# Optimization experiments

Measured on AMD Instinct MI355X. Metric: run time of the kernel, lower is better.

## Reference

```python
import jax, jax.numpy as jnp
import numpy as np


def setup_inputs() -> dict:
    key = jax.random.key(0)
    P, B, S = 128, 128, 4096
    k1, k2, k3, k4 = jax.random.split(key, 4)
    # SPD inducing Gram K_ii
    A = jax.random.normal(k1, (P, 2 * P), jnp.float32)
    K_ii = A @ A.T / (2.0 * P) + 1e-2 * jnp.eye(P, dtype=jnp.float32)
    # cross-covariances [B, S, P]
    K_ti = jax.random.normal(k2, (B, S, P), jnp.float32) * 0.1
    # diagonal K_t must dominate the quadratic form so the Schur complement is positive
    Kii_inv = jnp.linalg.inv(K_ii)
    qf = jnp.einsum('bsp,pq,bsq->bs', K_ti, Kii_inv, K_ti)
    K_t = qf + jax.random.uniform(k3, (B, S), jnp.float32) + 0.1
    # learned parameters
    V = jax.random.normal(k4, (P, P), jnp.float32) / jnp.sqrt(P) + jnp.eye(P, dtype=jnp.float32)
    latent_Gscale = jnp.zeros((), jnp.float32)
    dof = 128
    return dict(K_ii=K_ii, K_ti=K_ti, K_t=K_t, V=V, latent_Gscale=latent_Gscale, dof=dof)


def reference(K_ii, K_ti, K_t, V, latent_Gscale, dof):
    P = K_ii.shape[0]
    ti = K_ti.reshape(-1, P)          # [N, P]
    tt = K_t.reshape(-1)              # [N]
    # pos_inv via Cholesky (SPD inverse)
    L = jnp.linalg.cholesky(K_ii)
    Kii_inv = jax.scipy.linalg.cho_solve((L, True), jnp.eye(P, dtype=K_ii.dtype))
    A = ti @ Kii_inv                  # Kti_inv_Kii_flat, [N, P]
    ktt_i = tt - jnp.sum(A * ti, -1)  # Schur complement diag
    # G = V V^T / P * exp(scale)
    G = (V @ V.T) / V.shape[1] * jnp.exp(latent_Gscale)
    Gti = A @ G                       # [N, P]
    gt = jnp.sum(Gti * A, -1) + ktt_i
    # objective: -0.5 * dof * (-(logdet G + logdet Kinv) + tr(Kinv G) - P)
    trace_term = jnp.sum(Kii_inv * G.T)
    logdet_G = jnp.linalg.slogdet(G)[1]
    logdet_Kinv = -2.0 * jnp.sum(jnp.log(jnp.diag(L)))
    obj = -0.5 * dof * (-(logdet_G + logdet_Kinv) + trace_term - P)
    Gii = G
    return (Gii, Gti.reshape(K_ti.shape), gt.reshape(K_t.shape), obj)
```

## Files before the change

kernel.cpp:

```cpp
#include <hip/hip_runtime.h>
#include <cstdint>

typedef __attribute__((ext_vector_type(8))) short short8;
typedef __attribute__((ext_vector_type(4))) float f32x4;

__device__ __forceinline__ unsigned short f2bf(float f) {
    uint32_t u = __builtin_bit_cast(uint32_t, f);
    u += 0x7FFFu + ((u >> 16) & 1u);
    return (unsigned short)(u >> 16);
}

#define SG_OFF   16384
#define SM1_OFF  32768
#define SY_OFF   49152
#define SX_OFF   65536
#define SD_OFF   81920

__global__ __launch_bounds__(256) void k0_G(
    const float* __restrict__ V, const float* __restrict__ gs,
    float* __restrict__ out)
{
    float* sG = out + SG_OFF;
    const float egs = expf(gs[0]) * (1.0f / 128.0f);
    const int ty = threadIdx.x >> 5, tx = threadIdx.x & 31;
    const int r = blockIdx.x * 8 + ty;
    const f32x4* V4 = (const f32x4*)V;
    f32x4 acc = {0.f, 0.f, 0.f, 0.f};
    for (int kq = 0; kq < 32; ++kq) {
        const f32x4 vr = V4[r * 32 + kq];
        #pragma unroll
        for (int e = 0; e < 4; ++e) {
            const f32x4 vc = V4[(tx * 4 + e) * 32 + kq];
            acc[e] += vr[0]*vc[0] + vr[1]*vc[1] + vr[2]*vc[2] + vr[3]*vc[3];
        }
    }
    acc *= egs;
    *(f32x4*)&out[r * 128 + tx * 4] = acc;
    *(f32x4*)&sG[r * 128 + tx * 4] = acc;
}

__global__ __launch_bounds__(512) void k1_factor(
    const float* __restrict__ Kii, float* __restrict__ out)
{
    __shared__ float colA[2][128], colB[2][128], rowX[2][128];
    __shared__ float sDk[128], sDg[128], sRed[4];

    const int tid = threadIdx.x;
    const int ty = tid >> 5, tx = tid & 31;
    const int I0 = ty * 8, J0 = tx * 4;
    const float* sG = out + SG_OFF;
    float* sX = out + SX_OFF;
    float* dbuf = out + SD_OFF;

    f32x4 rA[8], rB[8], rX[8];
    #pragma unroll
    for (int r = 0; r < 8; ++r) {
        rA[r] = *(const f32x4*)&Kii[(size_t)(I0 + r) * 128 + J0];
        rB[r] = *(const f32x4*)&sG[(I0 + r) * 128 + J0];
        f32x4 z = {0.f, 0.f, 0.f, 0.f};
        #pragma unroll
        for (int e = 0; e < 4; ++e) z[e] = (I0 + r == J0 + e) ? 1.0f : 0.0f;
        rX[r] = z;
    }
    if (tx == 0) {
        #pragma unroll
        for (int r = 0; r < 8; ++r) { colA[0][I0 + r] = rA[r][0]; colB[0][I0 + r] = rB[r][0]; }
    }
    if (ty == 0) {
        #pragma unroll
        for (int e = 0; e < 4; ++e) rowX[0][J0 + e] = rX[0][e];
    }
    __syncthreads();

    for (int k = 0; k < 127; ++k) {
        const int b = k & 1;
        const float dK = colA[b][k], dG = colB[b][k];
        const float rdK = 1.0f / dK, rdG = 1.0f / dG;
        if (tid == 0) { sDk[k] = dK; sDg[k] = dG; }

        f32x4 caj = *(const f32x4*)&colA[b][J0];
        f32x4 cbj = *(const f32x4*)&colB[b][J0];
        const f32x4 xj = *(const f32x4*)&rowX[b][J0];
        #pragma unroll
        for (int e = 0; e < 4; ++e)
            if (J0 + e <= k) { caj[e] = 0.0f; cbj[e] = 0.0f; }

        f32x4 ca0 = *(const f32x4*)&colA[b][I0];
        f32x4 ca1 = *(const f32x4*)&colA[b][I0 + 4];
        f32x4 cb0 = *(const f32x4*)&colB[b][I0];
        f32x4 cb1 = *(const f32x4*)&colB[b][I0 + 4];
        #pragma unroll
        for (int r = 0; r < 4; ++r) {
            if (I0 + r <= k)     { ca0[r] = 0.0f; cb0[r] = 0.0f; }
            if (I0 + 4 + r <= k) { ca1[r] = 0.0f; cb1[r] = 0.0f; }
        }

        if (I0 + 7 > k) {
            #pragma unroll
            for (int r = 0; r < 8; ++r) {
                const float am = (r < 4) ? ca0[r & 3] : ca1[r & 3];
                const float bm = (r < 4) ? cb0[r & 3] : cb1[r & 3];
                const float fA = am * rdK;
                const float fB = bm * rdG;
                rA[r] -= fA * caj;
                rB[r] -= fB * cbj;
                rX[r] -= fA * xj;
            }
        }

        const int kn = k + 1, bn = kn & 1;
        if (tx == (kn >> 2)) {
            const int es = kn & 3;
            #pragma unroll
            for (int ee = 0; ee < 4; ++ee) if (ee == es) {
                #pragma unroll
                for (int r = 0; r < 8; ++r) {
                    colA[bn][I0 + r] = rA[r][ee];
                    colB[bn][I0 + r] = rB[r][ee];
                }
            }
        }
        if (ty == (kn >> 3)) {
            const int rs = kn & 7;
            #pragma unroll
            for (int rr = 0; rr < 8; ++rr) if (rr == rs) {
                #pragma unroll
                for (int e = 0; e < 4; ++e) rowX[bn][J0 + e] = rX[rr][e];
            }
        }
        __syncthreads();
    }
    if (tid == 511) { sDk[127] = rA[7][3]; sDg[127] = rB[7][3]; }

    #pragma unroll
    for (int r = 0; r < 8; ++r)
        *(f32x4*)&sX[(I0 + r) * 128 + J0] = rX[r];
    __syncthreads();

    if (tid < 128) {
        dbuf[tid] = sDk[tid];
        float lk = logf(sDk[tid]);
        float lg = logf(sDg[tid]);
        #pragma unroll
        for (int o = 32; o > 0; o >>= 1) { lk += __shfl_xor(lk, o, 64); lg += __shfl_xor(lg, o, 64); }
        if ((tid & 63) == 0) { sRed[(tid >> 6) * 2] = lk; sRed[(tid >> 6) * 2 + 1] = lg; }
    }
    __syncthreads();
    if (tid == 0) {
        dbuf[128] = sRed[0] + sRed[2];
        dbuf[129] = sRed[1] + sRed[3];
    }
}

__global__ __launch_bounds__(256) void k2_M1(float* __restrict__ out)
{
    const float* sX = out + SX_OFF;
    const float* dbuf = out + SD_OFF;
    float* sM1 = out + SM1_OFF;
    __shared__ float srd[128];
    const int tid = threadIdx.x;
    if (tid < 128) srd[tid] = 1.0f / dbuf[tid];
    __syncthreads();
    const int ty = tid >> 5, tx = tid & 31;
    const int a = blockIdx.x * 8 + ty;
    const f32x4* X4 = (const f32x4*)sX;
    f32x4 acc = {0.f, 0.f, 0.f, 0.f};
    for (int k = a; k < 128; ++k) {
        const float xa = sX[k * 128 + a] * srd[k];
        acc += xa * X4[k * 32 + tx];
    }
    *(f32x4*)&sM1[a * 128 + tx * 4] = acc;
}

__global__ __launch_bounds__(256) void k3_Y(float* __restrict__ out, char* __restrict__ wsb)
{
    const float* sG = out + SG_OFF;
    const float* sM1 = out + SM1_OFF;
    float* sY = out + SY_OFF;
    float* dbuf = out + SD_OFF;
    const int tid = threadIdx.x;
    const int ty = tid >> 5, tx = tid & 31;
    const int c = blockIdx.x * 8 + ty;
    const f32x4* M14 = (const f32x4*)sM1;
    f32x4 acc = {0.f, 0.f, 0.f, 0.f};
    for (int m = 0; m < 128; ++m)
        acc += sG[c * 128 + m] * M14[m * 32 + tx];
    *(f32x4*)&sY[c * 128 + tx * 4] = acc;
    const uint32_t lo = (uint32_t)f2bf(acc[0]) | ((uint32_t)f2bf(acc[1]) << 16);
    const uint32_t hi = (uint32_t)f2bf(acc[2]) | ((uint32_t)f2bf(acc[3]) << 16);
    const uint32_t byteoff = (uint32_t)((c * 256 + tx * 8) ^ ((c & 7) << 4));
    *(uint2*)(wsb + byteoff) = make_uint2(lo, hi);
    float t;
    {
        const f32x4* G4 = (const f32x4*)sG;
        const int idx = blockIdx.x * 256 + tid;
        const f32x4 g = G4[idx], mm = M14[idx];
        t = g[0]*mm[0] + g[1]*mm[1] + g[2]*mm[2] + g[3]*mm[3];
    }
    #pragma unroll
    for (int o = 32; o > 0; o >>= 1) t += __shfl_xor(t, o, 64);
    __shared__ float sp[4];
    if ((tid & 63) == 0) sp[tid >> 6] = t;
    __syncthreads();
    if (tid == 0) dbuf[132 + blockIdx.x] = sp[0] + sp[1] + sp[2] + sp[3];
}

__global__ __launch_bounds__(256) void k4_Q(
    float* __restrict__ out, char* __restrict__ wsb, const int* __restrict__ dofp)
{
    const float* sM1 = out + SM1_OFF;
    const float* sY = out + SY_OFF;
    const float* dbuf = out + SD_OFF;
    const int tid = threadIdx.x;
    const int ty = tid >> 5, tx = tid & 31;
    const int c = blockIdx.x * 8 + ty;
    const f32x4* Y4 = (const f32x4*)sY;
    const f32x4* M14 = (const f32x4*)sM1;
    f32x4 acc = -M14[c * 32 + tx];
    for (int m = 0; m < 128; ++m)
        acc += sM1[c * 128 + m] * Y4[m * 32 + tx];
    const uint32_t lo = (uint32_t)f2bf(acc[0]) | ((uint32_t)f2bf(acc[1]) << 16);
    const uint32_t hi = (uint32_t)f2bf(acc[2]) | ((uint32_t)f2bf(acc[3]) << 16);
    const uint32_t byteoff = (uint32_t)((c * 256 + tx * 8) ^ ((c & 7) << 4));
    *(uint2*)(wsb + 32768 + byteoff) = make_uint2(lo, hi);
    if (blockIdx.x == 0 && tid == 0) {
        float trace = 0.0f;
        for (int i = 0; i < 16; ++i) trace += dbuf[132 + i];
        const float ldK = dbuf[128], ldG = dbuf[129];
        const float dof = (float)dofp[0];
        out[67649536] = -0.5f * dof * (-(ldG - ldK) + trace - 128.0f);
    }
}

__global__ __launch_bounds__(512) void main_kernel(
    const float* __restrict__ Kti, const float* __restrict__ Kt,
    const float* __restrict__ ws, float* __restrict__ Gti,
    float* __restrict__ gt)
{
    __shared__ __align__(16) char smem[65536];
    const int tid = threadIdx.x;
    const int lane = tid & 63, wid = tid >> 6;
    const int l15 = lane & 15, l4 = lane >> 4;
    const int brow = blockIdx.x * 256;
    const int wrow = wid * 32;

    const float* tbase = Kti + (size_t)(brow + wrow + l15) * 128;

    f32x4 t[4][4];
    #pragma unroll
    for (int kc = 0; kc < 4; ++kc) {
        const float* p0 = tbase + kc * 32 + l4 * 8;
        const float* p1 = p0 + 16 * 128;
        t[kc][0] = *(const f32x4*)p0;
        t[kc][1] = *(const f32x4*)(p0 + 4);
        t[kc][2] = *(const f32x4*)p1;
        t[kc][3] = *(const f32x4*)(p1 + 4);
    }

    {
        f32x4* s4 = (f32x4*)smem;
        const f32x4* w4 = (const f32x4*)ws;
        #pragma unroll
        for (int i = 0; i < 8; ++i) s4[tid + i * 512] = w4[tid + i * 512];
    }

    short8 a[4][2];
    #pragma unroll
    for (int kc = 0; kc < 4; ++kc) {
        a[kc][0] = { (short)f2bf(t[kc][0][0]), (short)f2bf(t[kc][0][1]), (short)f2bf(t[kc][0][2]), (short)f2bf(t[kc][0][3]),
                     (short)f2bf(t[kc][1][0]), (short)f2bf(t[kc][1][1]), (short)f2bf(t[kc][1][2]), (short)f2bf(t[kc][1][3]) };
        a[kc][1] = { (short)f2bf(t[kc][2][0]), (short)f2bf(t[kc][2][1]), (short)f2bf(t[kc][2][2]), (short)f2bf(t[kc][2][3]),
                     (short)f2bf(t[kc][3][0]), (short)f2bf(t[kc][3][1]), (short)f2bf(t[kc][3][2]), (short)f2bf(t[kc][3][3]) };
    }
    __syncthreads();

    f32x4 accW[2][8] = {};
    f32x4 accZ[2][8] = {};
    #pragma unroll
    for (int kc = 0; kc < 4; ++kc) {
        const int k0 = kc * 32 + l4 * 8;
        #pragma unroll
        for (int ct = 0; ct < 8; ++ct) {
            const int c = ct * 16 + l15;
            const int byteoff = (c * 256 + k0 * 2) ^ ((c & 7) << 4);
            const short8 bW = *(const short8*)(smem + byteoff);
            const short8 bQ = *(const short8*)(smem + 32768 + byteoff);
            accW[0][ct] = __builtin_amdgcn_mfma_f32_16x16x32_bf16(a[kc][0], bW, accW[0][ct], 0, 0, 0);
            accW[1][ct] = __builtin_amdgcn_mfma_f32_16x16x32_bf16(a[kc][1], bW, accW[1][ct], 0, 0, 0);
            accZ[0][ct] = __builtin_amdgcn_mfma_f32_16x16x32_bf16(a[kc][0], bQ, accZ[0][ct], 0, 0, 0);
            accZ[1][ct] = __builtin_amdgcn_mfma_f32_16x16x32_bf16(a[kc][1], bQ, accZ[1][ct], 0, 0, 0);
        }
    }

    #pragma unroll
    for (int rt = 0; rt < 2; ++rt) {
        #pragma unroll
        for (int r = 0; r < 4; ++r) {
            const int row = brow + wrow + rt * 16 + l4 * 4 + r;
            const float* trow = Kti + (size_t)row * 128;
            float p = 0.0f;
            #pragma unroll
            for (int ct = 0; ct < 8; ++ct) p += accZ[rt][ct][r] * trow[ct * 16 + l15];
            p += __shfl_xor(p, 1, 64);
            p += __shfl_xor(p, 2, 64);
            p += __shfl_xor(p, 4, 64);
            p += __shfl_xor(p, 8, 64);
            if (l15 == 0) gt[row] = Kt[row] + p;
        }
    }

    #pragma unroll
    for (int rt = 0; rt < 2; ++rt) {
        #pragma unroll
        for (int r = 0; r < 4; ++r) {
            float* grow = Gti + (size_t)(brow + wrow + rt * 16 + l4 * 4 + r) * 128 + l15;
            #pragma unroll
            for (int ct = 0; ct < 8; ++ct)
                grow[ct * 16] = accW[rt][ct][r];
        }
    }
}

extern "C" void kernel_launch(void* const* d_in, const int* in_sizes, int n_in,
                              void* d_out, int out_size, void* d_ws, size_t ws_size,
                              hipStream_t stream)
{
    const float* Kii = (const float*)d_in[0];
    const float* Kti = (const float*)d_in[1];
    const float* Kt  = (const float*)d_in[2];
    const float* V   = (const float*)d_in[3];
    const float* gs  = (const float*)d_in[4];
    const int*   dof = (const int*)d_in[5];
    float* out = (float*)d_out;
    float* ws  = (float*)d_ws;

    const int N = in_sizes[2];
    const int nblocks = N / 256;

    k0_G<<<16, 256, 0, stream>>>(V, gs, out);
    k1_factor<<<1, 512, 0, stream>>>(Kii, out);
    k2_M1<<<16, 256, 0, stream>>>(out);
    k3_Y<<<16, 256, 0, stream>>>(out, (char*)ws);
    k4_Q<<<16, 256, 0, stream>>>(out, (char*)ws, dof);
    main_kernel<<<nblocks, 512, 0, stream>>>(Kti, Kt, ws,
                                             out + 16384,
                                             out + 67125248);
}
```

Before: 305.5 us.

## Make main kernel persistent with 128-row tiles and register prefetch of next tile

The main kernel becomes a persistent grid of 512 blocks that loop over 128-row tiles. Each wave now handles 16 rows instead of 32, which halves the accumulator registers, and launch bounds request 4 blocks per CU. The next tile's K_ti rows are prefetched into registers while the MFMAs for the current tile run, and the 64KB weight copy into LDS happens once per block instead of once per 256 rows. The risks are the LDS budget limiting real occupancy below the requested 4 blocks, and the smaller per-wave tile lowering MFMA density.

```diff
diff --git a/kernel.cpp b/kernel.cpp
--- a/kernel.cpp
+++ b/kernel.cpp
@@ -232,30 +232,16 @@
     }
 }
 
-__global__ __launch_bounds__(512) void main_kernel(
+__global__ __launch_bounds__(512, 4) void main_kernel(
     const float* __restrict__ Kti, const float* __restrict__ Kt,
     const float* __restrict__ ws, float* __restrict__ Gti,
-    float* __restrict__ gt)
+    float* __restrict__ gt, int ntiles)
 {
     __shared__ __align__(16) char smem[65536];
     const int tid = threadIdx.x;
     const int lane = tid & 63, wid = tid >> 6;
     const int l15 = lane & 15, l4 = lane >> 4;
-    const int brow = blockIdx.x * 256;
-    const int wrow = wid * 32;
-
-    const float* tbase = Kti + (size_t)(brow + wrow + l15) * 128;
-
-    f32x4 t[4][4];
-    #pragma unroll
-    for (int kc = 0; kc < 4; ++kc) {
-        const float* p0 = tbase + kc * 32 + l4 * 8;
-        const float* p1 = p0 + 16 * 128;
-        t[kc][0] = *(const f32x4*)p0;
-        t[kc][1] = *(const f32x4*)(p0 + 4);
-        t[kc][2] = *(const f32x4*)p1;
-        t[kc][3] = *(const f32x4*)(p1 + 4);
-    }
+    const int wrow = wid * 16;
 
     {
         f32x4* s4 = (f32x4*)smem;
@@ -264,60 +250,79 @@
         for (int i = 0; i < 8; ++i) s4[tid + i * 512] = w4[tid + i * 512];
     }
 
-    short8 a[4][2];
-    #pragma unroll
-    for (int kc = 0; kc < 4; ++kc) {
-        a[kc][0] = { (short)f2bf(t[kc][0][0]), (short)f2bf(t[kc][0][1]), (short)f2bf(t[kc][0][2]), (short)f2bf(t[kc][0][3]),
-                     (short)f2bf(t[kc][1][0]), (short)f2bf(t[kc][1][1]), (short)f2bf(t[kc][1][2]), (short)f2bf(t[kc][1][3]) };
-        a[kc][1] = { (short)f2bf(t[kc][2][0]), (short)f2bf(t[kc][2][1]), (short)f2bf(t[kc][2][2]), (short)f2bf(t[kc][2][3]),
-                     (short)f2bf(t[kc][3][0]), (short)f2bf(t[kc][3][1]), (short)f2bf(t[kc][3][2]), (short)f2bf(t[kc][3][3]) };
-    }
-    __syncthreads();
-
-    f32x4 accW[2][8] = {};
-    f32x4 accZ[2][8] = {};
-    #pragma unroll
-    for (int kc = 0; kc < 4; ++kc) {
-        const int k0 = kc * 32 + l4 * 8;
-        #pragma unroll
-        for (int ct = 0; ct < 8; ++ct) {
-            const int c = ct * 16 + l15;
-            const int byteoff = (c * 256 + k0 * 2) ^ ((c & 7) << 4);
-            const short8 bW = *(const short8*)(smem + byteoff);
-            const short8 bQ = *(const short8*)(smem + 32768 + byteoff);
-            accW[0][ct] = __builtin_amdgcn_mfma_f32_16x16x32_bf16(a[kc][0], bW, accW[0][ct], 0, 0, 0);
-            accW[1][ct] = __builtin_amdgcn_mfma_f32_16x16x32_bf16(a[kc][1], bW, accW[1][ct], 0, 0, 0);
-            accZ[0][ct] = __builtin_amdgcn_mfma_f32_16x16x32_bf16(a[kc][0], bQ, accZ[0][ct], 0, 0, 0);
-            accZ[1][ct] = __builtin_amdgcn_mfma_f32_16x16x32_bf16(a[kc][1], bQ, accZ[1][ct], 0, 0, 0);
-        }
-    }
-
-    #pragma unroll
-    for (int rt = 0; rt < 2; ++rt) {
+    int tile = blockIdx.x;
+    f32x4 t[4][2];
+    {
+        const float* tb = Kti + ((size_t)tile * 128 + wrow + l15) * 128 + l4 * 8;
+        #pragma unroll
+        for (int kc = 0; kc < 4; ++kc) {
+            t[kc][0] = *(const f32x4*)(tb + kc * 32);
+            t[kc][1] = *(const f32x4*)(tb + kc * 32 + 4);
+        }
+    }
+    __syncthreads();
+
+    while (tile < ntiles) {
+        const int curtile = tile;
+        const int nexttile = tile + gridDim.x;
+
+        short8 a[4];
+        #pragma unroll
+        for (int kc = 0; kc < 4; ++kc) {
+            a[kc] = { (short)f2bf(t[kc][0][0]), (short)f2bf(t[kc][0][1]),
+                      (short)f2bf(t[kc][0][2]), (short)f2bf(t[kc][0][3]),
+                      (short)f2bf(t[kc][1][0]), (short)f2bf(t[kc][1][1]),
+                      (short)f2bf(t[kc][1][2]), (short)f2bf(t[kc][1][3]) };
+        }
+
+        if (nexttile < ntiles) {
+            const float* tb = Kti + ((size_t)nexttile * 128 + wrow + l15) * 128 + l4 * 8;
+            #pragma unroll
+            for (int kc = 0; kc < 4; ++kc) {
+                t[kc][0] = *(const f32x4*)(tb + kc * 32);
+                t[kc][1] = *(const f32x4*)(tb + kc * 32 + 4);
+            }
+        }
+
+        f32x4 accW[8] = {};
+        f32x4 accZ[8] = {};
+        #pragma unroll
+        for (int kc = 0; kc < 4; ++kc) {
+            const int k0 = kc * 32 + l4 * 8;
+            #pragma unroll
+            for (int ct = 0; ct < 8; ++ct) {
+                const int c = ct * 16 + l15;
+                const int byteoff = (c * 256 + k0 * 2) ^ ((c & 7) << 4);
+                const short8 bW = *(const short8*)(smem + byteoff);
+                const short8 bQ = *(const short8*)(smem + 32768 + byteoff);
+                accW[ct] = __builtin_amdgcn_mfma_f32_16x16x32_bf16(a[kc], bW, accW[ct], 0, 0, 0);
+                accZ[ct] = __builtin_amdgcn_mfma_f32_16x16x32_bf16(a[kc], bQ, accZ[ct], 0, 0, 0);
+            }
+        }
+
         #pragma unroll
         for (int r = 0; r < 4; ++r) {
-            const int row = brow + wrow + rt * 16 + l4 * 4 + r;
+            const int row = curtile * 128 + wrow + l4 * 4 + r;
             const float* trow = Kti + (size_t)row * 128;
             float p = 0.0f;
             #pragma unroll
-            for (int ct = 0; ct < 8; ++ct) p += accZ[rt][ct][r] * trow[ct * 16 + l15];
+            for (int ct = 0; ct < 8; ++ct) p += accZ[ct][r] * trow[ct * 16 + l15];
             p += __shfl_xor(p, 1, 64);
             p += __shfl_xor(p, 2, 64);
             p += __shfl_xor(p, 4, 64);
             p += __shfl_xor(p, 8, 64);
             if (l15 == 0) gt[row] = Kt[row] + p;
         }
-    }
-
-    #pragma unroll
-    for (int rt = 0; rt < 2; ++rt) {
+
         #pragma unroll
         for (int r = 0; r < 4; ++r) {
-            float* grow = Gti + (size_t)(brow + wrow + rt * 16 + l4 * 4 + r) * 128 + l15;
+            float* grow = Gti + (size_t)(curtile * 128 + wrow + l4 * 4 + r) * 128 + l15;
             #pragma unroll
             for (int ct = 0; ct < 8; ++ct)
-                grow[ct * 16] = accW[rt][ct][r];
-        }
+                grow[ct * 16] = accW[ct][r];
+        }
+
+        tile = nexttile;
     }
 }
 
@@ -335,14 +340,15 @@
     float* ws  = (float*)d_ws;
 
     const int N = in_sizes[2];
-    const int nblocks = N / 256;
+    const int ntiles = N / 128;
 
     k0_G<<<16, 256, 0, stream>>>(V, gs, out);
     k1_factor<<<1, 512, 0, stream>>>(Kii, out);
     k2_M1<<<16, 256, 0, stream>>>(out);
     k3_Y<<<16, 256, 0, stream>>>(out, (char*)ws);
     k4_Q<<<16, 256, 0, stream>>>(out, (char*)ws, dof);
-    main_kernel<<<nblocks, 512, 0, stream>>>(Kti, Kt, ws,
-                                             out + 16384,
-                                             out + 67125248);
-}
+    main_kernel<<<512, 512, 0, stream>>>(Kti, Kt, ws,
+                                         out + 16384,
+                                         out + 67125248,
+                                         ntiles);
+}
```

New measurement: 869.9 us. 2.85x slower.

## Fuse M1, Y, Q setup kernels into the single-block factor kernel

Applied to the files above, without the earlier changes.

Merges the three small 16-block matrix-product kernels (M1, Y, Q) and the objective computation into the single-block Cholesky/inverse kernel, using block-wide syncthreads instead of kernel boundaries. This removes three kernel launches and their inter-kernel gaps. In exchange the 128x128 products run on one workgroup instead of 16, so the serial setup work per CU grows. The old kernel also computed M1 only for k >= a, while the fused loop sums over all k.

```diff
diff --git a/kernel.cpp b/kernel.cpp
--- a/kernel.cpp
+++ b/kernel.cpp
@@ -14,7 +14,6 @@
 #define SM1_OFF  32768
 #define SY_OFF   49152
 #define SX_OFF   65536
-#define SD_OFF   81920
 
 __global__ __launch_bounds__(256) void k0_G(
     const float* __restrict__ V, const float* __restrict__ gs,
@@ -39,18 +38,19 @@
     *(f32x4*)&sG[r * 128 + tx * 4] = acc;
 }
 
-__global__ __launch_bounds__(512) void k1_factor(
-    const float* __restrict__ Kii, float* __restrict__ out)
+__global__ __launch_bounds__(512) void kB_setup(
+    const float* __restrict__ Kii, const int* __restrict__ dofp,
+    float* __restrict__ out, char* __restrict__ wsb)
 {
     __shared__ float colA[2][128], colB[2][128], rowX[2][128];
-    __shared__ float sDk[128], sDg[128], sRed[4];
+    __shared__ float sDk[128], sDg[128], srd_s[128];
+    __shared__ float sRed[4], sTr[8], sLd[2], sTrTot;
 
     const int tid = threadIdx.x;
     const int ty = tid >> 5, tx = tid & 31;
     const int I0 = ty * 8, J0 = tx * 4;
     const float* sG = out + SG_OFF;
     float* sX = out + SX_OFF;
-    float* dbuf = out + SD_OFF;
 
     f32x4 rA[8], rB[8], rX[8];
     #pragma unroll
@@ -138,7 +138,7 @@
     __syncthreads();
 
     if (tid < 128) {
-        dbuf[tid] = sDk[tid];
+        srd_s[tid] = 1.0f / sDk[tid];
         float lk = logf(sDk[tid]);
         float lg = logf(sDg[tid]);
         #pragma unroll
@@ -147,88 +147,101 @@
     }
     __syncthreads();
     if (tid == 0) {
-        dbuf[128] = sRed[0] + sRed[2];
-        dbuf[129] = sRed[1] + sRed[3];
-    }
-}
-
-__global__ __launch_bounds__(256) void k2_M1(float* __restrict__ out)
-{
-    const float* sX = out + SX_OFF;
-    const float* dbuf = out + SD_OFF;
-    float* sM1 = out + SM1_OFF;
-    __shared__ float srd[128];
-    const int tid = threadIdx.x;
-    if (tid < 128) srd[tid] = 1.0f / dbuf[tid];
-    __syncthreads();
-    const int ty = tid >> 5, tx = tid & 31;
-    const int a = blockIdx.x * 8 + ty;
-    const f32x4* X4 = (const f32x4*)sX;
-    f32x4 acc = {0.f, 0.f, 0.f, 0.f};
-    for (int k = a; k < 128; ++k) {
-        const float xa = sX[k * 128 + a] * srd[k];
-        acc += xa * X4[k * 32 + tx];
-    }
-    *(f32x4*)&sM1[a * 128 + tx * 4] = acc;
-}
-
-__global__ __launch_bounds__(256) void k3_Y(float* __restrict__ out, char* __restrict__ wsb)
-{
-    const float* sG = out + SG_OFF;
-    const float* sM1 = out + SM1_OFF;
-    float* sY = out + SY_OFF;
-    float* dbuf = out + SD_OFF;
-    const int tid = threadIdx.x;
-    const int ty = tid >> 5, tx = tid & 31;
-    const int c = blockIdx.x * 8 + ty;
-    const f32x4* M14 = (const f32x4*)sM1;
-    f32x4 acc = {0.f, 0.f, 0.f, 0.f};
-    for (int m = 0; m < 128; ++m)
-        acc += sG[c * 128 + m] * M14[m * 32 + tx];
-    *(f32x4*)&sY[c * 128 + tx * 4] = acc;
-    const uint32_t lo = (uint32_t)f2bf(acc[0]) | ((uint32_t)f2bf(acc[1]) << 16);
-    const uint32_t hi = (uint32_t)f2bf(acc[2]) | ((uint32_t)f2bf(acc[3]) << 16);
-    const uint32_t byteoff = (uint32_t)((c * 256 + tx * 8) ^ ((c & 7) << 4));
-    *(uint2*)(wsb + byteoff) = make_uint2(lo, hi);
-    float t;
+        sLd[0] = sRed[0] + sRed[2];
+        sLd[1] = sRed[1] + sRed[3];
+    }
+    __syncthreads();
+
     {
-        const f32x4* G4 = (const f32x4*)sG;
-        const int idx = blockIdx.x * 256 + tid;
-        const f32x4 g = G4[idx], mm = M14[idx];
-        t = g[0]*mm[0] + g[1]*mm[1] + g[2]*mm[2] + g[3]*mm[3];
-    }
-    #pragma unroll
-    for (int o = 32; o > 0; o >>= 1) t += __shfl_xor(t, o, 64);
-    __shared__ float sp[4];
-    if ((tid & 63) == 0) sp[tid >> 6] = t;
-    __syncthreads();
-    if (tid == 0) dbuf[132 + blockIdx.x] = sp[0] + sp[1] + sp[2] + sp[3];
-}
-
-__global__ __launch_bounds__(256) void k4_Q(
-    float* __restrict__ out, char* __restrict__ wsb, const int* __restrict__ dofp)
-{
-    const float* sM1 = out + SM1_OFF;
-    const float* sY = out + SY_OFF;
-    const float* dbuf = out + SD_OFF;
-    const int tid = threadIdx.x;
-    const int ty = tid >> 5, tx = tid & 31;
-    const int c = blockIdx.x * 8 + ty;
-    const f32x4* Y4 = (const f32x4*)sY;
-    const f32x4* M14 = (const f32x4*)sM1;
-    f32x4 acc = -M14[c * 32 + tx];
-    for (int m = 0; m < 128; ++m)
-        acc += sM1[c * 128 + m] * Y4[m * 32 + tx];
-    const uint32_t lo = (uint32_t)f2bf(acc[0]) | ((uint32_t)f2bf(acc[1]) << 16);
-    const uint32_t hi = (uint32_t)f2bf(acc[2]) | ((uint32_t)f2bf(acc[3]) << 16);
-    const uint32_t byteoff = (uint32_t)((c * 256 + tx * 8) ^ ((c & 7) << 4));
-    *(uint2*)(wsb + 32768 + byteoff) = make_uint2(lo, hi);
-    if (blockIdx.x == 0 && tid == 0) {
-        float trace = 0.0f;
-        for (int i = 0; i < 16; ++i) trace += dbuf[132 + i];
-        const float ldK = dbuf[128], ldG = dbuf[129];
+        float* sM1 = out + SM1_OFF;
+        const float* sXg = sX;
+        f32x4 acc[8] = {};
+        for (int k = 0; k < 128; ++k) {
+            const f32x4 xv = *(const f32x4*)&sXg[k * 128 + tx * 4];
+            const float rd = srd_s[k];
+            const f32x4 xa0 = *(const f32x4*)&sXg[k * 128 + I0];
+            const f32x4 xa1 = *(const f32x4*)&sXg[k * 128 + I0 + 4];
+            #pragma unroll
+            for (int r = 0; r < 4; ++r) {
+                acc[r]     += (xa0[r] * rd) * xv;
+                acc[r + 4] += (xa1[r] * rd) * xv;
+            }
+        }
+        #pragma unroll
+        for (int r = 0; r < 8; ++r)
+            *(f32x4*)&sM1[(I0 + r) * 128 + tx * 4] = acc[r];
+    }
+    __syncthreads();
+
+    {
+        const float* sGg = out + SG_OFF;
+        const float* sM1 = out + SM1_OFF;
+        float* sY = out + SY_OFF;
+        const f32x4* M14 = (const f32x4*)sM1;
+        f32x4 acc[8] = {};
+        for (int m = 0; m < 128; ++m) {
+            const f32x4 mv = M14[m * 32 + tx];
+            #pragma unroll
+            for (int r = 0; r < 8; ++r)
+                acc[r] += sGg[(I0 + r) * 128 + m] * mv;
+        }
+        #pragma unroll
+        for (int r = 0; r < 8; ++r) {
+            const int c = I0 + r;
+            *(f32x4*)&sY[c * 128 + tx * 4] = acc[r];
+            const uint32_t lo = (uint32_t)f2bf(acc[r][0]) | ((uint32_t)f2bf(acc[r][1]) << 16);
+            const uint32_t hi = (uint32_t)f2bf(acc[r][2]) | ((uint32_t)f2bf(acc[r][3]) << 16);
+            const uint32_t byteoff = (uint32_t)((c * 256 + tx * 8) ^ ((c & 7) << 4));
+            *(uint2*)(wsb + byteoff) = make_uint2(lo, hi);
+        }
+        const f32x4* G4 = (const f32x4*)sGg;
+        float t = 0.0f;
+        #pragma unroll
+        for (int i = 0; i < 8; ++i) {
+            const int idx = tid + i * 512;
+            const f32x4 g = G4[idx], mm = M14[idx];
+            t += g[0]*mm[0] + g[1]*mm[1] + g[2]*mm[2] + g[3]*mm[3];
+        }
+        #pragma unroll
+        for (int o = 32; o > 0; o >>= 1) t += __shfl_xor(t, o, 64);
+        if ((tid & 63) == 0) sTr[tid >> 6] = t;
+    }
+    __syncthreads();
+    if (tid == 0) {
+        float tr = 0.0f;
+        #pragma unroll
+        for (int i = 0; i < 8; ++i) tr += sTr[i];
+        sTrTot = tr;
+    }
+    __syncthreads();
+
+    {
+        const float* sM1 = out + SM1_OFF;
+        const float* sY = out + SY_OFF;
+        const f32x4* Y4 = (const f32x4*)sY;
+        const f32x4* M14 = (const f32x4*)sM1;
+        f32x4 acc[8];
+        #pragma unroll
+        for (int r = 0; r < 8; ++r) acc[r] = -M14[(I0 + r) * 32 + tx];
+        for (int m = 0; m < 128; ++m) {
+            const f32x4 yv = Y4[m * 32 + tx];
+            #pragma unroll
+            for (int r = 0; r < 8; ++r)
+                acc[r] += sM1[(I0 + r) * 128 + m] * yv;
+        }
+        #pragma unroll
+        for (int r = 0; r < 8; ++r) {
+            const int c = I0 + r;
+            const uint32_t lo = (uint32_t)f2bf(acc[r][0]) | ((uint32_t)f2bf(acc[r][1]) << 16);
+            const uint32_t hi = (uint32_t)f2bf(acc[r][2]) | ((uint32_t)f2bf(acc[r][3]) << 16);
+            const uint32_t byteoff = (uint32_t)((c * 256 + tx * 8) ^ ((c & 7) << 4));
+            *(uint2*)(wsb + 32768 + byteoff) = make_uint2(lo, hi);
+        }
+    }
+    if (tid == 0) {
+        const float ldK = sLd[0], ldG = sLd[1];
         const float dof = (float)dofp[0];
-        out[67649536] = -0.5f * dof * (-(ldG - ldK) + trace - 128.0f);
+        out[67649536] = -0.5f * dof * (-(ldG - ldK) + sTrTot - 128.0f);
     }
 }
 
@@ -338,10 +351,7 @@
     const int nblocks = N / 256;
 
     k0_G<<<16, 256, 0, stream>>>(V, gs, out);
-    k1_factor<<<1, 512, 0, stream>>>(Kii, out);
-    k2_M1<<<16, 256, 0, stream>>>(out);
-    k3_Y<<<16, 256, 0, stream>>>(out, (char*)ws);
-    k4_Q<<<16, 256, 0, stream>>>(out, (char*)ws, dof);
+    kB_setup<<<1, 512, 0, stream>>>(Kii, dof, out, (char*)ws);
     main_kernel<<<nblocks, 512, 0, stream>>>(Kti, Kt, ws,
                                              out + 16384,
                                              out + 67125248);
```

Result: slower. 372.9 us (+22.1%).
